# Optimization experiments

Hardware: AMD Instinct MI355X
Metric: run time of the kernel (lower is better)

The kernel has to match this reference:

```python
import jax, jax.numpy as jnp
import numpy as np

HEADS = 16
LN_EPS = 1e-5


def setup_inputs() -> dict:
    key = jax.random.key(0)
    k0, k1, k2 = jax.random.split(key, 3)
    B, NE, D = 8, 2048, 1024
    qk_scale = np.sqrt(1.0 / D) * np.sqrt(2.0 / (D + 2 * D))  # xavier_normal gain sqrt(qk_w/D)
    v_scale = np.sqrt(0.01 / D) * np.sqrt(2.0 / (D + D))      # xavier_normal gain sqrt(v_w/D)
    return {
        "inp": jax.random.normal(k0, (B, NE, D), dtype=jnp.float32),
        "gamma": jnp.ones((D,), dtype=jnp.float32),
        "beta": jnp.zeros((D,), dtype=jnp.float32),
        "W_qk": jax.random.normal(k1, (D, 2 * D), dtype=jnp.float32) * qk_scale,
        "b_qk": jnp.zeros((2 * D,), dtype=jnp.float32),
        "W_v": jax.random.normal(k2, (D, D), dtype=jnp.float32) * v_scale,
        "b_v": jnp.zeros((D,), dtype=jnp.float32),
    }


def reference(inp, gamma, beta, W_qk, b_qk, W_v, b_v):
    B, NE, D = inp.shape
    hd = D // HEADS
    # LayerNorm over last dim
    mu = jnp.mean(inp, axis=-1, keepdims=True)
    var = jnp.mean(jnp.square(inp - mu), axis=-1, keepdims=True)
    x = (inp - mu) * jax.lax.rsqrt(var + LN_EPS) * gamma + beta
    # fused qk projection; note interleaved q/k layout in last axis of the view
    qk = (jnp.einsum("bnd,de->bne", x, W_qk) + b_qk).reshape(B, NE, HEADS, hd, 2)
    q = qk[..., 0]  # [B, NE, H, hd]
    k = qk[..., 1]
    v = (jnp.einsum("bnd,de->bne", x, W_v) + b_v).reshape(B, NE, HEADS, hd)
    q = jnp.transpose(q, (0, 2, 1, 3))  # [B, H, NE, hd]
    k = jnp.transpose(k, (0, 2, 3, 1))  # [B, H, hd, NE]
    v = jnp.transpose(v, (0, 2, 1, 3))  # [B, H, NE, hd]
    return (q, k, v)
```

## Files before the change

kernel.cpp:

```cpp
#include <hip/hip_runtime.h>
#include <hip/hip_bf16.h>

#define D_DIM 1024
#define M_TOT 16384
#define N_TOT 3072
#define NQK   2048
#define QKV_SZ 16777216

typedef __attribute__((ext_vector_type(8))) __bf16 bf16x8;
typedef __attribute__((ext_vector_type(4))) float floatx4;

__device__ __forceinline__ unsigned short f2bf(float f) {
  unsigned int u = __float_as_uint(f);
  u += 0x7FFFu + ((u >> 16) & 1u);
  return (unsigned short)(u >> 16);
}

__device__ __forceinline__ void gl2lds16(const void* g, void* l) {
  __builtin_amdgcn_global_load_lds(
      (const __attribute__((address_space(1))) void*)g,
      (__attribute__((address_space(3))) void*)l, 16, 0, 0);
}

__global__ __launch_bounds__(256) void ln_kernel(
    const float* __restrict__ inp, const float* __restrict__ gamma,
    const float* __restrict__ beta, unsigned short* __restrict__ X) {
  const int row = blockIdx.x;
  const int t = threadIdx.x;
  const float* rp = inp + (size_t)row * D_DIM;
  float4 v = *(const float4*)(rp + t * 4);
  float s  = v.x + v.y + v.z + v.w;
  float s2 = v.x * v.x + v.y * v.y + v.z * v.z + v.w * v.w;
#pragma unroll
  for (int o = 1; o < 64; o <<= 1) {
    s  += __shfl_xor(s, o);
    s2 += __shfl_xor(s2, o);
  }
  __shared__ float ws[8];
  const int w = t >> 6, l = t & 63;
  if (l == 0) { ws[w] = s; ws[4 + w] = s2; }
  __syncthreads();
  s  = ws[0] + ws[1] + ws[2] + ws[3];
  s2 = ws[4] + ws[5] + ws[6] + ws[7];
  const float mu = s * (1.0f / D_DIM);
  const float var = s2 * (1.0f / D_DIM) - mu * mu;
  const float rstd = rsqrtf(var + 1e-5f);
  float4 g = *(const float4*)(gamma + t * 4);
  float4 b = *(const float4*)(beta + t * 4);
  ushort4 o;
  o.x = f2bf((v.x - mu) * rstd * g.x + b.x);
  o.y = f2bf((v.y - mu) * rstd * g.y + b.y);
  o.z = f2bf((v.z - mu) * rstd * g.z + b.z);
  o.w = f2bf((v.w - mu) * rstd * g.w + b.w);
  *(ushort4*)(X + (size_t)row * D_DIM + t * 4) = o;
}

__global__ __launch_bounds__(256) void wt_kernel(
    const float* __restrict__ Wqk, const float* __restrict__ Wv,
    unsigned short* __restrict__ Wt) {
  __shared__ float tile[64][65];
  const int n0 = blockIdx.x * 64;
  const int k0 = blockIdx.y * 64;
  const float* src;
  int ldn, nc0;
  if (n0 < NQK) { src = Wqk; ldn = NQK; nc0 = n0; }
  else          { src = Wv;  ldn = D_DIM; nc0 = n0 - NQK; }
  const int t = threadIdx.x;
  const int r = t >> 4;
  const int c4 = (t & 15) << 2;
#pragma unroll
  for (int p = 0; p < 4; ++p) {
    int kk = p * 16 + r;
    float4 vv = *(const float4*)(src + (size_t)(k0 + kk) * ldn + nc0 + c4);
    tile[kk][c4 + 0] = vv.x;
    tile[kk][c4 + 1] = vv.y;
    tile[kk][c4 + 2] = vv.z;
    tile[kk][c4 + 3] = vv.w;
  }
  __syncthreads();
#pragma unroll
  for (int p = 0; p < 4; ++p) {
    int nn = p * 16 + r;
    ushort4 o;
    o.x = f2bf(tile[c4 + 0][nn]);
    o.y = f2bf(tile[c4 + 1][nn]);
    o.z = f2bf(tile[c4 + 2][nn]);
    o.w = f2bf(tile[c4 + 3][nn]);
    *(ushort4*)(Wt + (size_t)(n0 + nn) * D_DIM + k0 + c4) = o;
  }
}

__global__ __launch_bounds__(512, 2) void gemm_kernel(
    const unsigned short* __restrict__ X,
    const unsigned short* __restrict__ Wt,
    const float* __restrict__ bqk, const float* __restrict__ bv,
    float* __restrict__ out) {
  __shared__ __align__(16) unsigned char smem[131072];

  const int bid = blockIdx.x;
  const int xcd = bid & 7, tt = bid >> 3;
  const int bm = xcd * 8 + tt / 12;
  const int bn = tt % 12;
  const int m0 = bm * 256, n0 = bn * 256;

  const int tid = threadIdx.x;
  const int w = tid >> 6, l = tid & 63;
  const int wm = w >> 2, wn = w & 3;
  const int lr = l & 15, lg = l >> 4;

  const int rowL = w * 16 + (l >> 2);
  const int gcol = ((l & 3) ^ ((l >> 3) & 3)) * 8;
  const unsigned short* gA = X  + (size_t)(m0 + rowL) * D_DIM + gcol;
  const unsigned short* gB = Wt + (size_t)(n0 + rowL) * D_DIM + gcol;
  const int ldsW = w * 1024;

  floatx4 acc[8][4];
#pragma unroll
  for (int i = 0; i < 8; ++i)
#pragma unroll
    for (int j = 0; j < 4; ++j) acc[i][j] = (floatx4){0.f, 0.f, 0.f, 0.f};

#define STAGE(buf, ktn)                                                       \
  {                                                                           \
    const int kc_ = (ktn) * 32;                                               \
    unsigned char* base_ = smem + (buf) * 32768;                              \
    gl2lds16(gA + kc_,                       base_ + ldsW);                   \
    gl2lds16(gA + (size_t)128 * D_DIM + kc_, base_ + 8192 + ldsW);            \
    gl2lds16(gB + kc_,                       base_ + 16384 + ldsW);           \
    gl2lds16(gB + (size_t)128 * D_DIM + kc_, base_ + 24576 + ldsW);           \
  }

  STAGE(0, 0);
  STAGE(1, 1);
  STAGE(2, 2);

#pragma unroll 1
  for (int kt = 0; kt < 32; ++kt) {
    asm volatile("s_waitcnt vmcnt(8)" ::: "memory");
    __builtin_amdgcn_s_barrier();

    const unsigned char* Ab = smem + (kt & 3) * 32768;
    const unsigned char* Bb = Ab + 16384;

    bf16x8 bfr[4];
#pragma unroll
    for (int ni = 0; ni < 4; ++ni) {
      int off = (wn * 64 + ni * 16 + lr) * 64 + lg * 16;
      off ^= ((off >> 7) & 3) << 4;
      bfr[ni] = *(const bf16x8*)(Bb + off);
    }
    bf16x8 afr[8];
#pragma unroll
    for (int mi = 0; mi < 8; ++mi) {
      int off = (wm * 128 + mi * 16 + lr) * 64 + lg * 16;
      off ^= ((off >> 7) & 3) << 4;
      afr[mi] = *(const bf16x8*)(Ab + off);
    }

    STAGE((kt + 3) & 3, (kt + 3) & 31);

    __builtin_amdgcn_s_setprio(1);
#pragma unroll
    for (int mi = 0; mi < 8; ++mi)
#pragma unroll
      for (int ni = 0; ni < 4; ++ni)
        acc[mi][ni] = __builtin_amdgcn_mfma_f32_16x16x32_bf16(afr[mi], bfr[ni], acc[mi][ni], 0, 0, 0);
    __builtin_amdgcn_s_setprio(0);
  }
  asm volatile("s_waitcnt vmcnt(0)" ::: "memory");

  const size_t OQ = 0, OK = QKV_SZ, OV = 2 * (size_t)QKV_SZ;
  const int bb = m0 >> 11;
  const int mloc = m0 & 2047;
  float* Cf = (float*)smem;

#pragma unroll 1
  for (int pass = 0; pass < 4; ++pass) {
    __syncthreads();
    if (wn == pass) {
#pragma unroll
      for (int ni = 0; ni < 4; ++ni) {
        const int cl = ni * 16 + lr;
        const int ng = n0 + pass * 64 + cl;
        const float bias = (ng < NQK) ? bqk[ng] : bv[ng - NQK];
#pragma unroll
        for (int mi = 0; mi < 8; ++mi) {
          const int r0 = wm * 128 + mi * 16 + lg * 4;
#pragma unroll
          for (int j = 0; j < 4; ++j)
            Cf[(r0 + j) * 66 + cl] = acc[mi][ni][j] + bias;
        }
      }
    }
    __syncthreads();
    const int ng0 = n0 + pass * 64;
    if (ng0 < NQK) {
      const int h = ng0 >> 7;
      const int d0p = (ng0 & 127) >> 1;
      {
        const int row = tid >> 1, doff = (tid & 1) * 16;
        float* qp = out + OQ + (((size_t)(bb * 16 + h) * 2048 + mloc + row) * 64) + d0p + doff;
        float vb[16];
#pragma unroll
        for (int i = 0; i < 16; ++i) vb[i] = Cf[row * 66 + 2 * (doff + i)];
#pragma unroll
        for (int i4 = 0; i4 < 4; ++i4)
          *(float4*)(qp + i4 * 4) = make_float4(vb[i4*4], vb[i4*4+1], vb[i4*4+2], vb[i4*4+3]);
      }
      {
        const int dl = tid >> 4;
        const int neo = (tid & 15) * 16;
        float* kp = out + OK + (((size_t)(bb * 16 + h) * 64 + d0p + dl) * 2048) + mloc + neo;
        float vb[16];
#pragma unroll
        for (int i = 0; i < 16; ++i) vb[i] = Cf[(neo + i) * 66 + 2 * dl + 1];
#pragma unroll
        for (int i4 = 0; i4 < 4; ++i4)
          *(float4*)(kp + i4 * 4) = make_float4(vb[i4*4], vb[i4*4+1], vb[i4*4+2], vb[i4*4+3]);
      }
    } else {
      const int vbase = ng0 - NQK;
      const int h = vbase >> 6;
      const int row = tid >> 1, off = (tid & 1) * 32;
      float* vp = out + OV + (((size_t)(bb * 16 + h) * 2048 + mloc + row) * 64) + off;
#pragma unroll
      for (int i4 = 0; i4 < 8; ++i4) {
        float4 t4 = make_float4(Cf[row * 66 + off + i4*4],     Cf[row * 66 + off + i4*4 + 1],
                                Cf[row * 66 + off + i4*4 + 2], Cf[row * 66 + off + i4*4 + 3]);
        *(float4*)(vp + i4 * 4) = t4;
      }
    }
  }
#undef STAGE
}

extern "C" void kernel_launch(void* const* d_in, const int* in_sizes, int n_in,
                              void* d_out, int out_size, void* d_ws, size_t ws_size,
                              hipStream_t stream) {
  const float* inp   = (const float*)d_in[0];
  const float* gamma = (const float*)d_in[1];
  const float* beta  = (const float*)d_in[2];
  const float* Wqk   = (const float*)d_in[3];
  const float* bqk   = (const float*)d_in[4];
  const float* Wv    = (const float*)d_in[5];
  const float* bv    = (const float*)d_in[6];
  float* out = (float*)d_out;

  unsigned short* X  = (unsigned short*)d_ws;
  unsigned short* Wt = X + (size_t)M_TOT * D_DIM;

  ln_kernel<<<M_TOT, 256, 0, stream>>>(inp, gamma, beta, X);
  wt_kernel<<<dim3(N_TOT / 64, D_DIM / 64), 256, 0, stream>>>(Wqk, Wv, Wt);
  gemm_kernel<<<(M_TOT / 256) * (N_TOT / 256), 512, 0, stream>>>(X, Wt, bqk, bv, out);
}
```

Measured before the change: 400.6 us.

## Split GEMM k-step into two halves interleaving loads with MFMA, coalesce K-transpose stores

The main loop now issues the A prefetch, loads half of the A fragments and runs the first half of the MFMAs. It then issues the B prefetch, loads the second half of the A fragments and runs the rest, with a sched_barrier between the halves. This spreads global-to-LDS traffic and LDS reads across the MFMA work and lowers the number of A fragment registers live at once. The K-transpose epilogue also changes from 16 contiguous floats per thread to four float4s strided by 64, so stores from adjacent threads coalesce across a wavefront. The extra scheduling constraints may stop the compiler from overlapping as freely.

```diff
diff --git a/kernel.cpp b/kernel.cpp
--- a/kernel.cpp
+++ b/kernel.cpp
@@ -120,19 +120,24 @@
 #pragma unroll
     for (int j = 0; j < 4; ++j) acc[i][j] = (floatx4){0.f, 0.f, 0.f, 0.f};
 
-#define STAGE(buf, ktn)                                                       \
+#define STAGE_A(buf, ktn)                                                     \
   {                                                                           \
     const int kc_ = (ktn) * 32;                                               \
     unsigned char* base_ = smem + (buf) * 32768;                              \
     gl2lds16(gA + kc_,                       base_ + ldsW);                   \
     gl2lds16(gA + (size_t)128 * D_DIM + kc_, base_ + 8192 + ldsW);            \
+  }
+#define STAGE_B(buf, ktn)                                                     \
+  {                                                                           \
+    const int kc_ = (ktn) * 32;                                               \
+    unsigned char* base_ = smem + (buf) * 32768;                              \
     gl2lds16(gB + kc_,                       base_ + 16384 + ldsW);           \
     gl2lds16(gB + (size_t)128 * D_DIM + kc_, base_ + 24576 + ldsW);           \
   }
 
-  STAGE(0, 0);
-  STAGE(1, 1);
-  STAGE(2, 2);
+  STAGE_A(0, 0); STAGE_B(0, 0);
+  STAGE_A(1, 1); STAGE_B(1, 1);
+  STAGE_A(2, 2); STAGE_B(2, 2);
 
 #pragma unroll 1
   for (int kt = 0; kt < 32; ++kt) {
@@ -141,30 +146,45 @@
 
     const unsigned char* Ab = smem + (kt & 3) * 32768;
     const unsigned char* Bb = Ab + 16384;
-
-    bf16x8 bfr[4];
+    const int nbuf = (kt + 3) & 3, nkt = (kt + 3) & 31;
+
+    STAGE_A(nbuf, nkt);
+    bf16x8 bfr[4], afr[4];
 #pragma unroll
     for (int ni = 0; ni < 4; ++ni) {
       int off = (wn * 64 + ni * 16 + lr) * 64 + lg * 16;
       off ^= ((off >> 7) & 3) << 4;
       bfr[ni] = *(const bf16x8*)(Bb + off);
     }
-    bf16x8 afr[8];
-#pragma unroll
-    for (int mi = 0; mi < 8; ++mi) {
+#pragma unroll
+    for (int mi = 0; mi < 4; ++mi) {
       int off = (wm * 128 + mi * 16 + lr) * 64 + lg * 16;
       off ^= ((off >> 7) & 3) << 4;
       afr[mi] = *(const bf16x8*)(Ab + off);
     }
-
-    STAGE((kt + 3) & 3, (kt + 3) & 31);
-
     __builtin_amdgcn_s_setprio(1);
 #pragma unroll
-    for (int mi = 0; mi < 8; ++mi)
+    for (int mi = 0; mi < 4; ++mi)
 #pragma unroll
       for (int ni = 0; ni < 4; ++ni)
         acc[mi][ni] = __builtin_amdgcn_mfma_f32_16x16x32_bf16(afr[mi], bfr[ni], acc[mi][ni], 0, 0, 0);
+    __builtin_amdgcn_s_setprio(0);
+    __builtin_amdgcn_sched_barrier(0);
+
+    STAGE_B(nbuf, nkt);
+    bf16x8 afr2[4];
+#pragma unroll
+    for (int mi = 0; mi < 4; ++mi) {
+      int off = (wm * 128 + (mi + 4) * 16 + lr) * 64 + lg * 16;
+      off ^= ((off >> 7) & 3) << 4;
+      afr2[mi] = *(const bf16x8*)(Ab + off);
+    }
+    __builtin_amdgcn_s_setprio(1);
+#pragma unroll
+    for (int mi = 0; mi < 4; ++mi)
+#pragma unroll
+      for (int ni = 0; ni < 4; ++ni)
+        acc[mi + 4][ni] = __builtin_amdgcn_mfma_f32_16x16x32_bf16(afr2[mi], bfr[ni], acc[mi + 4][ni], 0, 0, 0);
     __builtin_amdgcn_s_setprio(0);
   }
   asm volatile("s_waitcnt vmcnt(0)" ::: "memory");
@@ -209,14 +229,17 @@
       }
       {
         const int dl = tid >> 4;
-        const int neo = (tid & 15) * 16;
-        float* kp = out + OK + (((size_t)(bb * 16 + h) * 64 + d0p + dl) * 2048) + mloc + neo;
-        float vb[16];
-#pragma unroll
-        for (int i = 0; i < 16; ++i) vb[i] = Cf[(neo + i) * 66 + 2 * dl + 1];
-#pragma unroll
-        for (int i4 = 0; i4 < 4; ++i4)
-          *(float4*)(kp + i4 * 4) = make_float4(vb[i4*4], vb[i4*4+1], vb[i4*4+2], vb[i4*4+3]);
+        const int L4 = (tid & 15) * 4;
+        float* kp = out + OK + (((size_t)(bb * 16 + h) * 64 + d0p + dl) * 2048) + mloc;
+#pragma unroll
+        for (int g = 0; g < 4; ++g) {
+          const int ne = L4 + 64 * g;
+          float4 t4 = make_float4(Cf[(ne + 0) * 66 + 2 * dl + 1],
+                                  Cf[(ne + 1) * 66 + 2 * dl + 1],
+                                  Cf[(ne + 2) * 66 + 2 * dl + 1],
+                                  Cf[(ne + 3) * 66 + 2 * dl + 1]);
+          *(float4*)(kp + ne) = t4;
+        }
       }
     } else {
       const int vbase = ng0 - NQK;
@@ -231,7 +254,8 @@
       }
     }
   }
-#undef STAGE
+#undef STAGE_A
+#undef STAGE_B
 }
 
 extern "C" void kernel_launch(void* const* d_in, const int* in_sizes, int n_in,
```

Measured after the change: 392.7 us. -2.0%, faster.
